# Optimization experiments

Measured on AMD Instinct MI355X. Metric: run time of the kernel, lower is better.

Reference implementation:

```python
import jax, jax.numpy as jnp
import numpy as np
from jax import lax

NUM_CLASSES = 10
NUM_ITERS = 3


def conv2d(x, w, b, stride):
    # x: [B,C,H,W], w: [O,I,kh,kw]
    y = lax.conv_general_dilated(x, w, (stride, stride), 'VALID',
                                 dimension_numbers=('NCHW', 'OIHW', 'NCHW'))
    return y + b[None, :, None, None]


def squash(t, axis=-1):
    sn = jnp.sum(t * t, axis=axis, keepdims=True)
    return (sn / (1.0 + sn)) * t / jnp.sqrt(sn)


def routing(x, W, num_iters=NUM_ITERS):
    # x: [B,R,Ci], W: [C,R,Ci,Co] -> outputs [B,C,Co]
    # priors[c,b,r,o] = sum_i x[b,r,i] * W[c,r,i,o]
    priors = jnp.einsum('bri,crio->cbro', x, W)  # [C,B,R,Co]
    C, B, R, Co = priors.shape
    # torch logits are [C,B,R,1,Co] but identical along Co (zeros init,
    # delta broadcast), so a [C,B,R,1] logit is mathematically identical.
    logits = jnp.zeros((C, B, R, 1), priors.dtype)
    outputs = None
    for i in range(num_iters):
        probs = jax.nn.softmax(logits, axis=2)            # over route nodes
        s = jnp.sum(probs * priors, axis=2, keepdims=True)  # [C,B,1,Co]
        outputs = squash(s, axis=-1)
        if i != num_iters - 1:
            logits = logits + jnp.sum(priors * outputs, axis=-1, keepdims=True)
    return jnp.transpose(outputs[:, :, 0, :], (1, 0, 2))  # [B,C,Co]


def setup_inputs() -> dict:
    key = jax.random.key(0)
    ks = jax.random.split(key, 16)
    B = 32
    s = 0.05
    inp = {
        'x': jax.random.normal(ks[0], (B, 1, 61, 61), jnp.float32),
        'conv0_w': jax.random.normal(ks[1], (256, 1, 9, 9), jnp.float32) * s,
        'conv0_b': jnp.zeros((256,), jnp.float32),
        'conv1_w': jax.random.normal(ks[2], (256, 256, 9, 9), jnp.float32) * s,
        'conv1_b': jnp.zeros((256,), jnp.float32),
        # 8 primary-capsule convs stacked: [8*32, 256, 9, 9]
        'prim_w': jax.random.normal(ks[3], (8 * 32, 256, 9, 9), jnp.float32) * s,
        'prim_b': jnp.zeros((8 * 32,), jnp.float32),
        'W1': jax.random.normal(ks[4], (64, 32 * 6 * 6, 8, 16), jnp.float32) * s,
        'W2': jax.random.normal(ks[5], (NUM_CLASSES, 64, 16, 16), jnp.float32) * s,
        'dec_w1': jax.random.normal(ks[6], (16 * NUM_CLASSES, 1024), jnp.float32) * s,
        'dec_b1': jnp.zeros((1024,), jnp.float32),
        'dec_w2': jax.random.normal(ks[7], (1024, 2048), jnp.float32) * s,
        'dec_b2': jnp.zeros((2048,), jnp.float32),
        'dec_w3': jax.random.normal(ks[8], (2048, 4096), jnp.float32) * s,
        'dec_b3': jnp.zeros((4096,), jnp.float32),
    }
    return inp


def reference(x, conv0_w, conv0_b, conv1_w, conv1_b, prim_w, prim_b,
              W1, W2, dec_w1, dec_b1, dec_w2, dec_b2, dec_w3, dec_b3):
    B = x.shape[0]
    h = jax.nn.relu(conv2d(x, conv0_w, conv0_b, 2))       # [B,256,27,27]
    h = jax.nn.relu(conv2d(h, conv1_w, conv1_b, 1))       # [B,256,19,19]
    # primary capsules: 8 convs of 32 channels each, k9 s2 -> [B,256,6,6]
    p = conv2d(h, prim_w, prim_b, 2)
    # torch: each capsule conv -> view(B, 32*6*6, 1), cat on last -> [B,1152,8]
    p = p.reshape(B, 8, 32 * 6 * 6)                        # [B,8,1152]
    p = jnp.transpose(p, (0, 2, 1))                        # [B,1152,8]
    p = squash(p, axis=-1)
    u = routing(p, W1)                                     # [B,64,16]
    v = routing(u, W2)                                     # [B,10,16]
    classes = jnp.sqrt(jnp.sum(v * v, axis=-1))            # [B,10]
    classes = jax.nn.softmax(classes, axis=-1)
    y = jax.nn.one_hot(jnp.argmax(classes, axis=1), NUM_CLASSES,
                       dtype=v.dtype)                       # [B,10]
    y = lax.stop_gradient(y)
    z = (v * y[:, :, None]).reshape(B, -1)                 # [B,160]
    d = jax.nn.relu(z @ dec_w1 + dec_b1)
    d = jax.nn.relu(d @ dec_w2 + dec_b2)
    reconstructions = jax.nn.sigmoid(d @ dec_w3 + dec_b3)  # [B,4096]
    return classes, reconstructions
```

## Files before the change

kernel.cpp:

```cpp
#include <hip/hip_runtime.h>
#include <hip/hip_bf16.h>
#include <math.h>


#define NB 32

typedef _Float16 f16;
typedef f16 f16x2 __attribute__((ext_vector_type(2)));
typedef f16 f16x4 __attribute__((ext_vector_type(4)));
typedef f16 f16x8 __attribute__((ext_vector_type(8)));
typedef float f32x4 __attribute__((ext_vector_type(4)));

__global__ void wprep_kernel(const float* __restrict__ w,
                             f16* __restrict__ wo) {
  for (int j = blockIdx.x * blockDim.x + threadIdx.x; j < 81 * 256 * 256;
       j += gridDim.x * blockDim.x) {
    int tap = j >> 16, rem = j & 65535;
    int oc = rem >> 8, ic = rem & 255;
    wo[j] = (f16)w[(oc * 256 + ic) * 81 + tap];
  }
}

__global__ __launch_bounds__(256) void conv0_kernel(
    const float* __restrict__ x, const float* __restrict__ w,
    const float* __restrict__ bias, f16* __restrict__ outf) {
  int b = blockIdx.x, ocg = blockIdx.y, z = blockIdx.z;
  __shared__ float img[61 * 61];
  __shared__ __align__(16) float wl[81][32];
  int t = threadIdx.x;
  for (int i = t; i < 61 * 61; i += 256) img[i] = x[b * 3721 + i];
  for (int i = t; i < 81 * 32; i += 256) {
    int k = i >> 5, oc = i & 31;
    wl[k][oc] = w[(ocg * 32 + oc) * 81 + k];
  }
  __syncthreads();
  int ocs = (t & 7) * 4;
  int pg  = t >> 3;
  int oc0 = ocg * 32 + ocs;
  float b0 = bias[oc0 + 0], b1 = bias[oc0 + 1], b2 = bias[oc0 + 2],
        b3 = bias[oc0 + 3];
  for (int p = pg + z * 32; p < 729; p += 64) {
    int oh = p / 27, ow = p - oh * 27;
    float a0 = 0.f, a1 = 0.f, a2 = 0.f, a3 = 0.f;
    const float* ib = &img[oh * 2 * 61 + ow * 2];
#pragma unroll
    for (int kh = 0; kh < 9; ++kh) {
#pragma unroll
      for (int kw = 0; kw < 9; ++kw) {
        float v = ib[kh * 61 + kw];
        const float4 wv =
            *reinterpret_cast<const float4*>(&wl[kh * 9 + kw][ocs]);
        a0 += v * wv.x; a1 += v * wv.y; a2 += v * wv.z; a3 += v * wv.w;
      }
    }
    int po = oh * 28 + ow;
    f16x4 hv;
    hv[0] = (f16)fmaxf(a0 + b0, 0.f);
    hv[1] = (f16)fmaxf(a1 + b1, 0.f);
    hv[2] = (f16)fmaxf(a2 + b2, 0.f);
    hv[3] = (f16)fmaxf(a3 + b3, 0.f);
    *(f16x4*)&outf[((size_t)b * 756 + po) * 256 + oc0] = hv;
  }
}

__global__ __launch_bounds__(256) void conv1_mfma(
    const f16* __restrict__ xin,
    const f16* __restrict__ wA,
    f16* __restrict__ part) {
  int b = blockIdx.x, ocg = blockIdx.y, ksp = blockIdx.z;
  __shared__ __align__(16) f16 blds[784 * 40];
  __shared__ __align__(16) f16 alds[64 * 40];
  int t = threadIdx.x;
  int w = t >> 6, lane = t & 63, kg = lane >> 4, ln = lane & 15;
  int pbB[6];
#pragma unroll
  for (int nf = 0; nf < 6; ++nf) {
    int n = w * 96 + nf * 16 + ln;
    int oh = n / 20, ow = n - oh * 20;
    pbB[nf] = ((oh * 28 + ow) * 40 + kg * 8) * 2;
  }
  int aoffB = (ln * 40 + kg * 8) * 2;
  f32x4 acc[4][6];
#pragma unroll
  for (int m = 0; m < 4; ++m)
#pragma unroll
    for (int nf = 0; nf < 6; ++nf) acc[m][nf] = (f32x4){0.f, 0.f, 0.f, 0.f};

  const f16* xb = xin + (size_t)b * 756 * 256 + ksp * 64;
  for (int icc = 0; icc < 2; ++icc) {
    __syncthreads();
    for (int i = t; i < 784 * 4; i += 256) {
      int p28 = i >> 2, q = i & 3;
      int p = (p28 < 756) ? p28 : (p28 - 28);
      f16x8 v = *(const f16x8*)(xb + (size_t)p * 256 + icc * 32 + q * 8);
      *(f16x8*)&blds[p28 * 40 + q * 8] = v;
    }
    for (int tap = 0; tap < 81; ++tap) {
      __syncthreads();
      {
        int oc = t >> 2, q = t & 3;
        f16x8 v = *(const f16x8*)(wA +
            ((size_t)tap * 256 + ocg * 64 + oc) * 256 + ksp * 64 +
            icc * 32 + q * 8);
        *(f16x8*)&alds[oc * 40 + q * 8] = v;
      }
      __syncthreads();
      int kh = tap / 9, kw = tap - kh * 9;
      int rowB = (kh * 28 + kw) * 80;
      f16x8 af[4];
#pragma unroll
      for (int m = 0; m < 4; ++m)
        af[m] = *(const f16x8*)((const char*)alds + m * (16 * 80) + aoffB);
      f16x8 bf[6];
#pragma unroll
      for (int nf = 0; nf < 6; ++nf)
        bf[nf] = *(const f16x8*)((const char*)blds + pbB[nf] + rowB);
#pragma unroll
      for (int m = 0; m < 4; ++m)
#pragma unroll
        for (int nf = 0; nf < 6; ++nf)
          acc[m][nf] = __builtin_amdgcn_mfma_f32_16x16x32_f16(
              af[m], bf[nf], acc[m][nf], 0, 0, 0);
    }
  }
  f16* pout = part + ((size_t)ksp * 32 + b) * 384 * 256 + ocg * 64;
#pragma unroll
  for (int m = 0; m < 4; ++m)
#pragma unroll
    for (int nf = 0; nf < 6; ++nf) {
      int n = w * 96 + nf * 16 + ln;
      int oc = m * 16 + kg * 4;
      f16x4 v;
#pragma unroll
      for (int j = 0; j < 4; ++j) v[j] = (f16)acc[m][nf][j];
      *(f16x4*)(pout + (size_t)n * 256 + oc) = v;
    }
}

__global__ void comb1_kernel(const f16* __restrict__ part,
                             const float* __restrict__ bias,
                             f16* __restrict__ h1f) {
  int idx = blockIdx.x * 256 + threadIdx.x;
  if (idx >= 32 * 380 * 32) return;
  int ocq = idx & 31, rem = idx >> 5;
  int p = rem % 380, b = rem / 380;
  float a[8];
#pragma unroll
  for (int j = 0; j < 8; ++j) a[j] = bias[ocq * 8 + j];
#pragma unroll
  for (int k = 0; k < 4; ++k) {
    f16x8 v = *(const f16x8*)&part[(((size_t)k * 32 + b) * 384 + p) * 256 +
                                   ocq * 8];
#pragma unroll
    for (int j = 0; j < 8; ++j) a[j] += (float)v[j];
  }
  f16x8 o;
#pragma unroll
  for (int j = 0; j < 8; ++j) o[j] = (f16)fmaxf(a[j], 0.f);
  *(f16x8*)&h1f[((size_t)b * 380 + p) * 256 + ocq * 8] = o;
}

__global__ __launch_bounds__(256) void prim_mfma(
    const f16* __restrict__ xin,
    const f16* __restrict__ wB,
    float* __restrict__ part2) {
  int ip = blockIdx.x, ocg = blockIdx.y, ksp = blockIdx.z;
  __shared__ __align__(16) f16 blds[768 * 40];
  __shared__ __align__(16) f16 alds[128 * 40];
  int t = threadIdx.x;
  int w = t >> 6, lane = t & 63, kg = lane >> 4, ln = lane & 15;
  int mg = w >> 1, ng = w & 1;
  int pb[3];
#pragma unroll
  for (int nf = 0; nf < 3; ++nf) {
    int rem = nf * 16 + ln;
    int oh6 = rem >> 3, ow6 = rem & 7;
    pb[nf] = ng * 384 + oh6 * 40 + ow6 * 2;
  }
  f32x4 acc[4][3];
#pragma unroll
  for (int m = 0; m < 4; ++m)
#pragma unroll
    for (int nf = 0; nf < 3; ++nf) acc[m][nf] = (f32x4){0.f, 0.f, 0.f, 0.f};

  for (int i = t; i < 768 * 4; i += 256) {
    int pos = i >> 2, q = i & 3;
    int img = pos >= 384;
    int p = pos - img * 384;
    if (p >= 380) p -= 20;
    f16x8 v = *(const f16x8*)(xin +
        ((size_t)(ip * 2 + img) * 380 + p) * 256 + ksp * 32 + q * 8);
    *(f16x8*)&blds[pos * 40 + q * 8] = v;
  }
  for (int tap = 0; tap < 81; ++tap) {
    __syncthreads();
    for (int i = t; i < 512; i += 256) {
      int oc = i >> 2, q = i & 3;
      f16x8 v = *(const f16x8*)(wB +
          ((size_t)tap * 256 + ocg * 128 + oc) * 256 + ksp * 32 + q * 8);
      *(f16x8*)&alds[oc * 40 + q * 8] = v;
    }
    __syncthreads();
    int kh = tap / 9, kw = tap - kh * 9;
    int shift = kh * 20 + kw;
    f16x8 af[4];
#pragma unroll
    for (int m = 0; m < 4; ++m)
      af[m] = *(const f16x8*)((const char*)alds +
                              (((mg * 4 + m) * 16 + ln) * 40 + kg * 8) * 2);
    f16x8 bf[3];
#pragma unroll
    for (int nf = 0; nf < 3; ++nf)
      bf[nf] = *(const f16x8*)((const char*)blds +
                               ((pb[nf] + shift) * 40 + kg * 8) * 2);
#pragma unroll
    for (int m = 0; m < 4; ++m)
#pragma unroll
      for (int nf = 0; nf < 3; ++nf)
        acc[m][nf] = __builtin_amdgcn_mfma_f32_16x16x32_f16(
            af[m], bf[nf], acc[m][nf], 0, 0, 0);
  }
  float* pout = part2 + ((size_t)ksp * 16 + ip) * 96 * 256 + ocg * 128;
#pragma unroll
  for (int m = 0; m < 4; ++m)
#pragma unroll
    for (int nf = 0; nf < 3; ++nf) {
      int n = ng * 48 + nf * 16 + ln;
      int oc = (mg * 4 + m) * 16 + kg * 4;
      *(f32x4*)(pout + (size_t)n * 256 + oc) = acc[m][nf];
    }
}

__global__ void comb2_kernel(const float* __restrict__ part2,
                             float* __restrict__ sum2) {
  int idx = blockIdx.x * 256 + threadIdx.x;
  if (idx >= 16 * 96 * 256) return;
  float a = 0.f;
#pragma unroll
  for (int k = 0; k < 8; ++k) a += part2[(size_t)k * 393216 + idx];
  sum2[idx] = a;
}

__global__ void prim_squash_kernel(const float* __restrict__ sum2,
                                   const float* __restrict__ bias,
                                   float* __restrict__ caps) {
  int idx = blockIdx.x * blockDim.x + threadIdx.x;
  if (idx >= NB * 1152) return;
  int b = idx / 1152, r = idx - b * 1152;
  int m = r / 36, s = r - m * 36;
  int oh6 = s / 6, ow6 = s - oh6 * 6;
  int n = (b & 1) * 48 + oh6 * 8 + ow6;
  const float* src = sum2 + ((size_t)(b >> 1) * 96 + n) * 256;
  float tv[8];
  float sn = 0.f;
#pragma unroll
  for (int g = 0; g < 8; ++g) {
    float v = src[g * 32 + m] + bias[g * 32 + m];
    tv[g] = v;
    sn += v * v;
  }
  float sc = sqrtf(sn) / (1.f + sn);
#pragma unroll
  for (int g = 0; g < 8; ++g) caps[idx * 8 + g] = tv[g] * sc;
}

__global__ __launch_bounds__(256) void priors1_kernel(
    const float* __restrict__ x,
    const float* __restrict__ W,
    f16* __restrict__ pri) {
  int c = blockIdx.x, rt = blockIdx.y;
  int r0 = rt * 32;
  __shared__ __align__(16) float xl[32 * 32 * 8];
  int t = threadIdx.x;
  for (int q = t; q < 2048; q += 256) {
    int b = q >> 6, j = q & 63;
    *(float4*)&xl[b * 256 + j * 4] =
        *(const float4*)&x[(size_t)b * 9216 + r0 * 8 + j * 4];
  }
  int rl = t >> 3, oq = t & 7;
  float w0[8], w1[8];
#pragma unroll
  for (int i = 0; i < 8; ++i) {
    const float2 wv = *(const float2*)&W[
        (((size_t)c * 1152 + r0 + rl) * 8 + i) * 16 + 2 * oq];
    w0[i] = wv.x; w1[i] = wv.y;
  }
  __syncthreads();
  f16* pout = pri + (size_t)c * 32 * 18432 + (r0 + rl) * 16 + 2 * oq;
#pragma unroll 4
  for (int b = 0; b < 32; ++b) {
    const float4 x0 = *(const float4*)&xl[b * 256 + rl * 8];
    const float4 x1 = *(const float4*)&xl[b * 256 + rl * 8 + 4];
    float s0 = x0.x * w0[0] + x0.y * w0[1] + x0.z * w0[2] + x0.w * w0[3] +
               x1.x * w0[4] + x1.y * w0[5] + x1.z * w0[6] + x1.w * w0[7];
    float s1 = x0.x * w1[0] + x0.y * w1[1] + x0.z * w1[2] + x0.w * w1[3] +
               x1.x * w1[4] + x1.y * w1[5] + x1.z * w1[6] + x1.w * w1[7];
    f16x2 hv; hv[0] = (f16)s0; hv[1] = (f16)s1;
    *(f16x2*)(pout + (size_t)b * 18432) = hv;
  }
}

__global__ __launch_bounds__(512) void route1_kernel(
    const f16* __restrict__ pri,
    float* __restrict__ out) {
  constexpr int R = 1152;
  constexpr int NREG = 36;
  int c = blockIdx.x, b = blockIdx.y;
  __shared__ float lg[R], pr[R];
  __shared__ float redA[8], redB[8];
  __shared__ float sred[8][16];
  __shared__ float vsh[17];
  int t    = threadIdx.x;
  int o    = t & 15;
  int rhi  = t >> 4;
  int wid  = t >> 6;
  int lane = t & 63;
  const f16* pb = pri + ((size_t)c * 32 + b) * (R * 16);

  float prireg[NREG];
#pragma unroll
  for (int k = 0; k < NREG; ++k)
    prireg[k] = (float)pb[(k * 32 + rhi) * 16 + o];
  for (int r = t; r < R; r += 512) lg[r] = 0.f;
  __syncthreads();

  for (int it = 0; it < 3; ++it) {
    float lm = -1e30f;
    for (int r = t; r < R; r += 512) lm = fmaxf(lm, lg[r]);
#pragma unroll
    for (int s2 = 1; s2 <= 32; s2 <<= 1) lm = fmaxf(lm, __shfl_xor(lm, s2));
    if (lane == 0) redA[wid] = lm;
    __syncthreads();
    if (t == 0) {
      float m8 = redA[0];
#pragma unroll
      for (int w = 1; w < 8; ++w) m8 = fmaxf(m8, redA[w]);
      redA[0] = m8;
    }
    __syncthreads();
    float m = redA[0];
    float ls = 0.f;
    for (int r = t; r < R; r += 512) {
      float e = __expf(lg[r] - m);
      pr[r] = e;
      ls += e;
    }
#pragma unroll
    for (int s2 = 1; s2 <= 32; s2 <<= 1) ls += __shfl_xor(ls, s2);
    if (lane == 0) redB[wid] = ls;
    __syncthreads();
    if (t == 0) {
      float s8 = 0.f;
#pragma unroll
      for (int w = 0; w < 8; ++w) s8 += redB[w];
      redB[0] = s8;
    }
    __syncthreads();
    float denom = redB[0];
    float part = 0.f;
#pragma unroll
    for (int k = 0; k < NREG; ++k) part += pr[k * 32 + rhi] * prireg[k];
    part += __shfl_xor(part, 16);
    part += __shfl_xor(part, 32);
    if (lane < 16) sred[wid][lane] = part;
    __syncthreads();
    if (t < 16) {
      float sv = 0.f;
#pragma unroll
      for (int w = 0; w < 8; ++w) sv += sred[w][t];
      vsh[t] = sv / denom;
    }
    __syncthreads();
    if (t == 0) {
      float sn = 0.f;
#pragma unroll
      for (int oo = 0; oo < 16; ++oo) sn += vsh[oo] * vsh[oo];
      vsh[16] = sqrtf(sn) / (1.f + sn);
    }
    __syncthreads();
    if (it < 2) {
      float vo = vsh[o] * vsh[16];
#pragma unroll
      for (int k = 0; k < NREG; ++k) {
        float val = prireg[k] * vo;
        val += __shfl_xor(val, 1);
        val += __shfl_xor(val, 2);
        val += __shfl_xor(val, 4);
        val += __shfl_xor(val, 8);
        if (o == 0) lg[k * 32 + rhi] += val;
      }
      __syncthreads();
    }
  }
  if (t < 16) out[((size_t)b * 64 + c) * 16 + t] = vsh[t] * vsh[16];
}

template <int R, int CI>
__global__ __launch_bounds__(512) void routing_kernel(
    const float* __restrict__ x,
    const float* __restrict__ W,
    float* __restrict__ out) {
  constexpr int NREG = R * 16 / 512;
  int c = blockIdx.x, b = blockIdx.y;
  int C = gridDim.x;
  __shared__ float xls[R * CI];
  extern __shared__ float rdyn[];
  float* lg = rdyn;
  float* pr = rdyn + R;
  __shared__ float redA[8], redB[8];
  __shared__ float sred[8][16];
  __shared__ float vsh[17];
  int t    = threadIdx.x;
  int o    = t & 15;
  int rhi  = t >> 4;
  int wid  = t >> 6;
  int lane = t & 63;
  const float* xb = x + (size_t)b * R * CI;
  const float* Wc = W + (size_t)c * R * CI * 16;

  for (int i = t; i < R * CI; i += 512) xls[i] = xb[i];
  for (int r = t; r < R; r += 512) lg[r] = 0.f;
  __syncthreads();

  float pri[NREG];
#pragma unroll
  for (int k = 0; k < NREG; ++k) {
    int r = k * 32 + rhi;
    float s = 0.f;
#pragma unroll
    for (int i = 0; i < CI; ++i)
      s += xls[r * CI + i] * Wc[((size_t)r * CI + i) * 16 + o];
    pri[k] = s;
  }

  for (int it = 0; it < 3; ++it) {
    float lm = -1e30f;
    for (int r = t; r < R; r += 512) lm = fmaxf(lm, lg[r]);
#pragma unroll
    for (int s2 = 1; s2 <= 32; s2 <<= 1) lm = fmaxf(lm, __shfl_xor(lm, s2));
    if (lane == 0) redA[wid] = lm;
    __syncthreads();
    if (t == 0) {
      float m8 = redA[0];
#pragma unroll
      for (int w = 1; w < 8; ++w) m8 = fmaxf(m8, redA[w]);
      redA[0] = m8;
    }
    __syncthreads();
    float m = redA[0];
    float ls = 0.f;
    for (int r = t; r < R; r += 512) {
      float e = __expf(lg[r] - m);
      pr[r] = e;
      ls += e;
    }
#pragma unroll
    for (int s2 = 1; s2 <= 32; s2 <<= 1) ls += __shfl_xor(ls, s2);
    if (lane == 0) redB[wid] = ls;
    __syncthreads();
    if (t == 0) {
      float s8 = 0.f;
#pragma unroll
      for (int w = 0; w < 8; ++w) s8 += redB[w];
      redB[0] = s8;
    }
    __syncthreads();
    float denom = redB[0];
    float part = 0.f;
#pragma unroll
    for (int k = 0; k < NREG; ++k) part += pr[k * 32 + rhi] * pri[k];
    part += __shfl_xor(part, 16);
    part += __shfl_xor(part, 32);
    if (lane < 16) sred[wid][lane] = part;
    __syncthreads();
    if (t < 16) {
      float sv = 0.f;
#pragma unroll
      for (int w = 0; w < 8; ++w) sv += sred[w][t];
      vsh[t] = sv / denom;
    }
    __syncthreads();
    if (t == 0) {
      float sn = 0.f;
#pragma unroll
      for (int oo = 0; oo < 16; ++oo) sn += vsh[oo] * vsh[oo];
      vsh[16] = sqrtf(sn) / (1.f + sn);
    }
    __syncthreads();
    if (it < 2) {
      float vo = vsh[o] * vsh[16];
#pragma unroll
      for (int k = 0; k < NREG; ++k) {
        float val = pri[k] * vo;
        val += __shfl_xor(val, 1);
        val += __shfl_xor(val, 2);
        val += __shfl_xor(val, 4);
        val += __shfl_xor(val, 8);
        if (o == 0) lg[k * 32 + rhi] += val;
      }
      __syncthreads();
    }
  }
  if (t < 16) out[((size_t)b * C + c) * 16 + t] = vsh[t] * vsh[16];
}

__global__ void classes_kernel(const float* __restrict__ v,
                               float* __restrict__ outc,
                               int* __restrict__ amaxb) {
  int b = blockIdx.x;
  int t = threadIdx.x;
  __shared__ float nrm[10];
  if (t < 10) {
    float sn = 0.f;
#pragma unroll
    for (int o = 0; o < 16; ++o) {
      float xv = v[(b * 10 + t) * 16 + o];
      sn += xv * xv;
    }
    nrm[t] = sqrtf(sn);
  }
  __syncthreads();
  if (t == 0) {
    float m = nrm[0];
    int am = 0;
    for (int c = 1; c < 10; ++c)
      if (nrm[c] > m) { m = nrm[c]; am = c; }
    float s = 0.f;
    float e[10];
    for (int c = 0; c < 10; ++c) { e[c] = __expf(nrm[c] - m); s += e[c]; }
    for (int c = 0; c < 10; ++c) outc[b * 10 + c] = e[c] / s;
    amaxb[b] = am;
  }
}

__global__ __launch_bounds__(256) void fc1s_kernel(
    const float* __restrict__ v, const int* __restrict__ amaxb,
    const float* __restrict__ w, const float* __restrict__ bias,
    float* __restrict__ out) {
  int n  = blockIdx.x * 256 + threadIdx.x;
  int b0 = blockIdx.y * 8;
  __shared__ float vls[8][16];
  __shared__ int ams[8];
  int t = threadIdx.x;
  if (t < 8) ams[t] = amaxb[b0 + t];
  __syncthreads();
  if (t < 128) {
    int bb = t >> 4, oo = t & 15;
    vls[bb][oo] = v[((b0 + bb) * 10 + ams[bb]) * 16 + oo];
  }
  __syncthreads();
  float bv = bias[n];
#pragma unroll
  for (int bb = 0; bb < 8; ++bb) {
    int row0 = ams[bb] * 16;
    float acc = bv;
#pragma unroll
    for (int oo = 0; oo < 16; ++oo)
      acc += vls[bb][oo] * w[(size_t)(row0 + oo) * 1024 + n];
    out[(size_t)(b0 + bb) * 1024 + n] = fmaxf(acc, 0.f);
  }
}

template <int K, int KCH>
__global__ __launch_bounds__(256) void fcsplit_kernel(
    const float* __restrict__ in, const float* __restrict__ w,
    float* __restrict__ pbuf, int N) {
  int n  = blockIdx.x * 256 + threadIdx.x;
  int b0 = blockIdx.y * 8;
  int k0 = blockIdx.z * KCH;
  __shared__ __align__(16) float inl[KCH * 8];
  for (int idx = threadIdx.x; idx < 8 * KCH; idx += 256) {
    int bb = idx / KCH, k = idx - bb * KCH;
    inl[k * 8 + bb] = in[(size_t)(b0 + bb) * K + k0 + k];
  }
  __syncthreads();
  float acc[8];
#pragma unroll
  for (int bb = 0; bb < 8; ++bb) acc[bb] = 0.f;
  for (int k = 0; k < KCH; ++k) {
    float wv = w[(size_t)(k0 + k) * N + n];
    const float4 i0 = *reinterpret_cast<const float4*>(&inl[k * 8]);
    const float4 i1 = *reinterpret_cast<const float4*>(&inl[k * 8 + 4]);
    acc[0] += i0.x * wv; acc[1] += i0.y * wv;
    acc[2] += i0.z * wv; acc[3] += i0.w * wv;
    acc[4] += i1.x * wv; acc[5] += i1.y * wv;
    acc[6] += i1.z * wv; acc[7] += i1.w * wv;
  }
#pragma unroll
  for (int bb = 0; bb < 8; ++bb)
    pbuf[((size_t)blockIdx.z * 32 + b0 + bb) * N + n] = acc[bb];
}

template <int KS, bool RELU, bool SIG>
__global__ void fccomb_kernel(const float* __restrict__ pbuf,
                              const float* __restrict__ bias,
                              float* __restrict__ out, int N) {
  int idx = blockIdx.x * 256 + threadIdx.x;
  if (idx >= 32 * N) return;
  int b = idx / N, n = idx - b * N;
  float a = bias[n];
#pragma unroll
  for (int kz = 0; kz < KS; ++kz) a += pbuf[((size_t)kz * 32 + b) * N + n];
  if (RELU) a = fmaxf(a, 0.f);
  if (SIG)  a = 1.f / (1.f + __expf(-a));
  out[idx] = a;
}

extern "C" void kernel_launch(void* const* d_in, const int* in_sizes, int n_in,
                              void* d_out, int out_size, void* d_ws,
                              size_t ws_size, hipStream_t stream) {
  const float* x       = (const float*)d_in[0];
  const float* conv0_w = (const float*)d_in[1];
  const float* conv0_b = (const float*)d_in[2];
  const float* conv1_w = (const float*)d_in[3];
  const float* conv1_b = (const float*)d_in[4];
  const float* prim_w  = (const float*)d_in[5];
  const float* prim_b  = (const float*)d_in[6];
  const float* W1      = (const float*)d_in[7];
  const float* W2      = (const float*)d_in[8];
  const float* dec_w1  = (const float*)d_in[9];
  const float* dec_b1  = (const float*)d_in[10];
  const float* dec_w2  = (const float*)d_in[11];
  const float* dec_b2  = (const float*)d_in[12];
  const float* dec_w3  = (const float*)d_in[13];
  const float* dec_b3  = (const float*)d_in[14];
  float* out = (float*)d_out;

  float* ws    = (float*)d_ws;
  float* caps  = ws;
  float* u     = caps + 294912;
  float* vc    = u + 32768;
  int*   amaxb = (int*)(vc + 5120);
  float* trans = vc + 5120 + 32;

  f16* wA    = (f16*)trans;
  f16* wB    = wA + 5308416;
  f16* h0f   = wB + 5308416;
  f16* h1f   = h0f + 6193152;
  f16* part1 = h1f + 3112960;
  float* part2 = (float*)part1;
  float* sum2  = part2 + 3145728;
  f16* pri1  = (f16*)trans;
  float* d1  = trans;
  float* d2  = d1 + 32768;
  float* pb2 = d2 + 65536;
  float* pb3 = pb2 + 262144;

  wprep_kernel<<<2048, 256, 0, stream>>>(conv1_w, wA);
  wprep_kernel<<<2048, 256, 0, stream>>>(prim_w, wB);

  conv0_kernel<<<dim3(NB, 8, 2), 256, 0, stream>>>(x, conv0_w, conv0_b, h0f);

  conv1_mfma<<<dim3(NB, 4, 4), 256, 0, stream>>>(h0f, wA, part1);
  comb1_kernel<<<1520, 256, 0, stream>>>(part1, conv1_b, h1f);

  prim_mfma<<<dim3(16, 2, 8), 256, 0, stream>>>(h1f, wB, part2);
  comb2_kernel<<<1536, 256, 0, stream>>>(part2, sum2);

  prim_squash_kernel<<<(NB * 1152 + 255) / 256, 256, 0, stream>>>(sum2, prim_b,
                                                                  caps);

  priors1_kernel<<<dim3(64, 36), 256, 0, stream>>>(caps, W1, pri1);
  route1_kernel<<<dim3(64, NB), 512, 0, stream>>>(pri1, u);

  routing_kernel<64, 16>
      <<<dim3(10, NB), 512, 2 * 64 * sizeof(float), stream>>>(u, W2, vc);

  classes_kernel<<<NB, 64, 0, stream>>>(vc, out, amaxb);

  fc1s_kernel<<<dim3(4, 4), 256, 0, stream>>>(vc, amaxb, dec_w1, dec_b1, d1);

  fcsplit_kernel<1024, 256>
      <<<dim3(8, 4, 4), 256, 0, stream>>>(d1, dec_w2, pb2, 2048);
  fccomb_kernel<4, true, false>
      <<<256, 256, 0, stream>>>(pb2, dec_b2, d2, 2048);

  fcsplit_kernel<2048, 256>
      <<<dim3(16, 4, 8), 256, 0, stream>>>(d2, dec_w3, pb3, 4096);
  fccomb_kernel<8, false, true>
      <<<512, 256, 0, stream>>>(pb3, dec_b3, out + 320, 4096);
}
```

Baseline: 511.2 us.

## Load MFMA A-operands straight from global with register prefetch, swizzle B LDS

In the conv1 and primary-capsule MFMA kernels, the per-tap weight tile is no longer staged through shared memory with two barriers per tap. Each lane now loads its A fragments directly from global memory, prefetching the next tap's fragments into registers one tap ahead. The B tile in LDS drops the padding in favour of an XOR swizzle, and launch bounds request two blocks per CU. The weight-prep kernel is rewritten so each thread transposes all 81 taps for one (oc,ic) pair, with a smaller grid. The per-tap loop no longer syncs, but the prefetch reads one tap past the end of the weights and global-load latency is now exposed per wave.

```diff
diff --git a/kernel.cpp b/kernel.cpp
--- a/kernel.cpp
+++ b/kernel.cpp
@@ -11,14 +11,18 @@
 typedef f16 f16x8 __attribute__((ext_vector_type(8)));
 typedef float f32x4 __attribute__((ext_vector_type(4)));
 
-__global__ void wprep_kernel(const float* __restrict__ w,
-                             f16* __restrict__ wo) {
-  for (int j = blockIdx.x * blockDim.x + threadIdx.x; j < 81 * 256 * 256;
-       j += gridDim.x * blockDim.x) {
-    int tap = j >> 16, rem = j & 65535;
-    int oc = rem >> 8, ic = rem & 255;
-    wo[j] = (f16)w[(oc * 256 + ic) * 81 + tap];
-  }
+__device__ __forceinline__ int swz(int row, int q) {
+  return row * 64 + ((q * 16) ^ (((row >> 1) & 3) << 4));
+}
+
+__global__ __launch_bounds__(256) void wprep_kernel(const float* __restrict__ w,
+                                                    f16* __restrict__ wo) {
+  int idx = blockIdx.x * 256 + threadIdx.x;
+  int oc = idx >> 8, ic = idx & 255;
+  const float* src = w + (size_t)(oc * 256 + ic) * 81;
+  f16* dst = wo + oc * 256 + ic;
+  for (int tap = 0; tap < 81; ++tap)
+    dst[(size_t)tap * 65536] = (f16)src[tap];
 }
 
 __global__ __launch_bounds__(256) void conv0_kernel(
@@ -63,23 +67,21 @@
   }
 }
 
-__global__ __launch_bounds__(256) void conv1_mfma(
+__global__ __launch_bounds__(256, 2) void conv1_mfma(
     const f16* __restrict__ xin,
     const f16* __restrict__ wA,
     f16* __restrict__ part) {
   int b = blockIdx.x, ocg = blockIdx.y, ksp = blockIdx.z;
-  __shared__ __align__(16) f16 blds[784 * 40];
-  __shared__ __align__(16) f16 alds[64 * 40];
+  __shared__ __align__(16) f16 blds[784 * 32];
   int t = threadIdx.x;
   int w = t >> 6, lane = t & 63, kg = lane >> 4, ln = lane & 15;
-  int pbB[6];
+  int prow[6];
 #pragma unroll
   for (int nf = 0; nf < 6; ++nf) {
     int n = w * 96 + nf * 16 + ln;
     int oh = n / 20, ow = n - oh * 20;
-    pbB[nf] = ((oh * 28 + ow) * 40 + kg * 8) * 2;
-  }
-  int aoffB = (ln * 40 + kg * 8) * 2;
+    prow[nf] = oh * 28 + ow;
+  }
   f32x4 acc[4][6];
 #pragma unroll
   for (int m = 0; m < 4; ++m)
@@ -87,40 +89,40 @@
     for (int nf = 0; nf < 6; ++nf) acc[m][nf] = (f32x4){0.f, 0.f, 0.f, 0.f};
 
   const f16* xb = xin + (size_t)b * 756 * 256 + ksp * 64;
+  const f16* abase = wA + (size_t)(ocg * 64 + ln) * 256 + ksp * 64 + kg * 8;
   for (int icc = 0; icc < 2; ++icc) {
     __syncthreads();
-    for (int i = t; i < 784 * 4; i += 256) {
+    for (int i = t; i < 3136; i += 256) {
       int p28 = i >> 2, q = i & 3;
       int p = (p28 < 756) ? p28 : (p28 - 28);
       f16x8 v = *(const f16x8*)(xb + (size_t)p * 256 + icc * 32 + q * 8);
-      *(f16x8*)&blds[p28 * 40 + q * 8] = v;
-    }
+      *(f16x8*)((char*)blds + swz(p28, q)) = v;
+    }
+    const f16* ap = abase + icc * 32;
+    f16x8 aN[4];
+#pragma unroll
+    for (int m = 0; m < 4; ++m) aN[m] = *(const f16x8*)(ap + m * 4096);
+    __syncthreads();
+#pragma unroll 3
     for (int tap = 0; tap < 81; ++tap) {
-      __syncthreads();
-      {
-        int oc = t >> 2, q = t & 3;
-        f16x8 v = *(const f16x8*)(wA +
-            ((size_t)tap * 256 + ocg * 64 + oc) * 256 + ksp * 64 +
-            icc * 32 + q * 8);
-        *(f16x8*)&alds[oc * 40 + q * 8] = v;
-      }
-      __syncthreads();
+      f16x8 aC[4];
+#pragma unroll
+      for (int m = 0; m < 4; ++m) aC[m] = aN[m];
+      const f16* apn = ap + (size_t)(tap + 1) * 65536;
+#pragma unroll
+      for (int m = 0; m < 4; ++m) aN[m] = *(const f16x8*)(apn + m * 4096);
       int kh = tap / 9, kw = tap - kh * 9;
-      int rowB = (kh * 28 + kw) * 80;
-      f16x8 af[4];
-#pragma unroll
-      for (int m = 0; m < 4; ++m)
-        af[m] = *(const f16x8*)((const char*)alds + m * (16 * 80) + aoffB);
+      int shift = kh * 28 + kw;
       f16x8 bf[6];
 #pragma unroll
       for (int nf = 0; nf < 6; ++nf)
-        bf[nf] = *(const f16x8*)((const char*)blds + pbB[nf] + rowB);
+        bf[nf] = *(const f16x8*)((const char*)blds + swz(prow[nf] + shift, kg));
 #pragma unroll
       for (int m = 0; m < 4; ++m)
 #pragma unroll
         for (int nf = 0; nf < 6; ++nf)
           acc[m][nf] = __builtin_amdgcn_mfma_f32_16x16x32_f16(
-              af[m], bf[nf], acc[m][nf], 0, 0, 0);
+              aC[m], bf[nf], acc[m][nf], 0, 0, 0);
     }
   }
   f16* pout = part + ((size_t)ksp * 32 + b) * 384 * 256 + ocg * 64;
@@ -160,22 +162,21 @@
   *(f16x8*)&h1f[((size_t)b * 380 + p) * 256 + ocq * 8] = o;
 }
 
-__global__ __launch_bounds__(256) void prim_mfma(
+__global__ __launch_bounds__(256, 2) void prim_mfma(
     const f16* __restrict__ xin,
     const f16* __restrict__ wB,
     float* __restrict__ part2) {
   int ip = blockIdx.x, ocg = blockIdx.y, ksp = blockIdx.z;
-  __shared__ __align__(16) f16 blds[768 * 40];
-  __shared__ __align__(16) f16 alds[128 * 40];
+  __shared__ __align__(16) f16 blds[768 * 32];
   int t = threadIdx.x;
   int w = t >> 6, lane = t & 63, kg = lane >> 4, ln = lane & 15;
   int mg = w >> 1, ng = w & 1;
-  int pb[3];
+  int rbase[3];
 #pragma unroll
   for (int nf = 0; nf < 3; ++nf) {
     int rem = nf * 16 + ln;
     int oh6 = rem >> 3, ow6 = rem & 7;
-    pb[nf] = ng * 384 + oh6 * 40 + ow6 * 2;
+    rbase[nf] = ng * 384 + oh6 * 40 + ow6 * 2;
   }
   f32x4 acc[4][3];
 #pragma unroll
@@ -183,42 +184,41 @@
 #pragma unroll
     for (int nf = 0; nf < 3; ++nf) acc[m][nf] = (f32x4){0.f, 0.f, 0.f, 0.f};
 
-  for (int i = t; i < 768 * 4; i += 256) {
+  for (int i = t; i < 3072; i += 256) {
     int pos = i >> 2, q = i & 3;
-    int img = pos >= 384;
+    int img = pos >= 384 ? 1 : 0;
     int p = pos - img * 384;
     if (p >= 380) p -= 20;
     f16x8 v = *(const f16x8*)(xin +
         ((size_t)(ip * 2 + img) * 380 + p) * 256 + ksp * 32 + q * 8);
-    *(f16x8*)&blds[pos * 40 + q * 8] = v;
-  }
+    *(f16x8*)((char*)blds + swz(pos, q)) = v;
+  }
+  const f16* abase =
+      wB + (size_t)(ocg * 128 + mg * 64 + ln) * 256 + ksp * 32 + kg * 8;
+  f16x8 aN[4];
+#pragma unroll
+  for (int m = 0; m < 4; ++m) aN[m] = *(const f16x8*)(abase + m * 4096);
+  __syncthreads();
+#pragma unroll 3
   for (int tap = 0; tap < 81; ++tap) {
-    __syncthreads();
-    for (int i = t; i < 512; i += 256) {
-      int oc = i >> 2, q = i & 3;
-      f16x8 v = *(const f16x8*)(wB +
-          ((size_t)tap * 256 + ocg * 128 + oc) * 256 + ksp * 32 + q * 8);
-      *(f16x8*)&alds[oc * 40 + q * 8] = v;
-    }
-    __syncthreads();
+    f16x8 aC[4];
+#pragma unroll
+    for (int m = 0; m < 4; ++m) aC[m] = aN[m];
+    const f16* apn = abase + (size_t)(tap + 1) * 65536;
+#pragma unroll
+    for (int m = 0; m < 4; ++m) aN[m] = *(const f16x8*)(apn + m * 4096);
     int kh = tap / 9, kw = tap - kh * 9;
     int shift = kh * 20 + kw;
-    f16x8 af[4];
-#pragma unroll
-    for (int m = 0; m < 4; ++m)
-      af[m] = *(const f16x8*)((const char*)alds +
-                              (((mg * 4 + m) * 16 + ln) * 40 + kg * 8) * 2);
     f16x8 bf[3];
 #pragma unroll
     for (int nf = 0; nf < 3; ++nf)
-      bf[nf] = *(const f16x8*)((const char*)blds +
-                               ((pb[nf] + shift) * 40 + kg * 8) * 2);
+      bf[nf] = *(const f16x8*)((const char*)blds + swz(rbase[nf] + shift, kg));
 #pragma unroll
     for (int m = 0; m < 4; ++m)
 #pragma unroll
       for (int nf = 0; nf < 3; ++nf)
         acc[m][nf] = __builtin_amdgcn_mfma_f32_16x16x32_f16(
-            af[m], bf[nf], acc[m][nf], 0, 0, 0);
+            aC[m], bf[nf], acc[m][nf], 0, 0, 0);
   }
   float* pout = part2 + ((size_t)ksp * 16 + ip) * 96 * 256 + ocg * 128;
 #pragma unroll
@@ -646,8 +646,8 @@
   float* pb2 = d2 + 65536;
   float* pb3 = pb2 + 262144;
 
-  wprep_kernel<<<2048, 256, 0, stream>>>(conv1_w, wA);
-  wprep_kernel<<<2048, 256, 0, stream>>>(prim_w, wB);
+  wprep_kernel<<<256, 256, 0, stream>>>(conv1_w, wA);
+  wprep_kernel<<<256, 256, 0, stream>>>(prim_w, wB);
 
   conv0_kernel<<<dim3(NB, 8, 2), 256, 0, stream>>>(x, conv0_w, conv0_b, h0f);
 
```

Result: faster. 484.7 us (-5.2%).
